# Kernel optimization log

Hardware: AMD Instinct MI355X
Metric: run time of the kernel (lower is better)

The kernel has to match this reference:

```python
import jax, jax.numpy as jnp
import numpy as np

B, L, C, N, TN = 1, 256, 128, 4, 4
CH = N * C  # 512, flattened hidden for routing projections
EPS = 1.1920929e-07  # torch.finfo(float32).eps (RMSNorm default eps)
LN_EPS = 1e-5
N_SINKHORN = 20  # training-mode iteration count


def sinkhorn_knopp(raw, n_iters):
    # raw: [..., n, n] real-valued logits -> doubly-stochastic matrix
    M = jnp.exp(raw)
    for _ in range(n_iters):
        M = M / jnp.sum(M, axis=-1, keepdims=True)  # row normalize
        M = M / jnp.sum(M, axis=-2, keepdims=True)  # col normalize
    return M


def setup_inputs() -> dict:
    key = jax.random.key(0)
    ks = jax.random.split(key, 8)
    s = 0.02
    eye = jnp.eye(N, dtype=jnp.float32)
    b_res = 2.0 * eye + (-2.0) * (1.0 - eye)
    return {
        "p": jax.random.normal(ks[0], (B, L, L, C), jnp.float32),
        "p_mask": jnp.ones((B, L, L), jnp.float32),
        "W_pre": jax.random.normal(ks[1], (N, CH), jnp.float32) * s,
        "W_post": jax.random.normal(ks[2], (N, CH), jnp.float32) * s,
        "W_res": jax.random.normal(ks[3], (N * N, CH), jnp.float32) * s,
        "b_pre": jnp.zeros((1, N), jnp.float32),
        "b_post": jnp.zeros((1, N), jnp.float32),
        "b_res": b_res,
        "alpha_pre": jnp.asarray(0.01, jnp.float32),
        "alpha_post": jnp.asarray(0.01, jnp.float32),
        "alpha_res": jnp.asarray(0.01, jnp.float32),
        "ln_g": jnp.ones((C,), jnp.float32),
        "ln_b": jnp.zeros((C,), jnp.float32),
        "W1": jax.random.normal(ks[4], (TN * C, C), jnp.float32) * s,
        "b1": jnp.zeros((TN * C,), jnp.float32),
        "W2": jax.random.normal(ks[5], (C, TN * C), jnp.float32) * s,
        "b2": jnp.zeros((C,), jnp.float32),
    }


def reference(p, p_mask, W_pre, W_post, W_res, b_pre, b_post, b_res,
              alpha_pre, alpha_post, alpha_res, ln_g, ln_b, W1, b1, W2, b2):
    # expand_input: [B,L,L,C] -> [B,L,L,n,C]
    x = jnp.broadcast_to(p[..., None, :], (B, L, L, N, C))
    # --- compute_mappings ---
    xf = x.reshape(B, L, L, CH)
    xn = xf * jax.lax.rsqrt(jnp.mean(xf * xf, axis=-1, keepdims=True) + EPS)
    H_pre_dyn = jnp.tanh(xn @ W_pre.T)                      # [B,L,L,n]
    H_post_dyn = jnp.tanh(xn @ W_post.T)                    # [B,L,L,n]
    H_res_dyn = jnp.tanh(xn @ W_res.T).reshape(B, L, L, N, N)
    H_pre = jax.nn.sigmoid(alpha_pre * H_pre_dyn + b_pre)   # [B,L,L,n]
    H_post = 2.0 * jax.nn.sigmoid(alpha_post * H_post_dyn + b_post)
    H_res = sinkhorn_knopp(alpha_res * H_res_dyn + b_res, N_SINKHORN)  # [B,L,L,n,n]
    # contract: H_pre [B,L,L,1,n] @ x [B,L,L,n,C] -> [B,L,L,C]
    p_c = jnp.einsum('blkn,blknc->blkc', H_pre, x)
    # --- PairTransition (LN -> Linear -> ReLU -> Linear, masked) ---
    mu = jnp.mean(p_c, axis=-1, keepdims=True)
    var = jnp.mean(jnp.square(p_c - mu), axis=-1, keepdims=True)
    m = (p_c - mu) * jax.lax.rsqrt(var + LN_EPS) * ln_g + ln_b
    h = jax.nn.relu(m @ W1.T + b1)                          # [B,L,L,TN*C]
    p_t = (h @ W2.T + b2) * p_mask[..., None]
    p_updated = p_c + p_t
    # expand back: H_post^T [B,L,L,n,1] * p_updated [B,L,L,1,C]
    p_expanded = H_post[..., :, None] * p_updated[..., None, :]
    # residual mixing: [B,L,L,n,n] @ [B,L,L,n,C]
    p_residual = jnp.einsum('blkmn,blknc->blkmc', H_res, x)
    return p_residual + p_expanded  # [B,L,L,n,C]
```

## Files before the change

kernel.cpp:

```cpp
#include <hip/hip_runtime.h>
#include <stdint.h>

#define LLTOT 65536
#define CDIM  128
#define TPIX  32

typedef float f32x4 __attribute__((ext_vector_type(4)));
typedef short s16x8 __attribute__((ext_vector_type(8)));

#define MFMA16(a, b, c) __builtin_amdgcn_mfma_f32_16x16x32_bf16((a), (b), (c), 0, 0, 0)

__device__ __align__(16) unsigned short g_wefff[2 * 4 * 64 * 8];
__device__ __align__(16) unsigned short g_w1gf[32 * 4 * 64 * 8];
__device__ __align__(16) unsigned short g_w2f [8 * 16 * 64 * 8];
__device__ __align__(16) float  g_hA[512];
__device__ __align__(16) float  g_w1gs[512];

__device__ __forceinline__ unsigned short f2bf(float f) {
    union { float f; uint32_t u; } v; v.f = f;
    uint32_t u = v.u;
    return (unsigned short)((u + 0x7FFFu + ((u >> 16) & 1u)) >> 16);
}
__device__ __forceinline__ uint32_t pack2(float a, float b) {
    uint32_t r;
    asm("v_cvt_pk_bf16_f32 %0, %1, %2" : "=v"(r) : "v"(a), "v"(b));
    return r;
}
__device__ __forceinline__ float bf2f(uint32_t lo16) { return __uint_as_float(lo16 << 16); }

__device__ __forceinline__ float fast_tanh(float x) {
    float cx = fminf(fmaxf(x, -10.f), 10.f);
    float e = __expf(2.f * cx);
    return (e - 1.f) * __builtin_amdgcn_rcpf(e + 1.f);
}
__device__ __forceinline__ float fast_sig(float z) {
    return __builtin_amdgcn_rcpf(1.f + __expf(-z));
}

__global__ void prep_kernel(const float* __restrict__ Wpre, const float* __restrict__ Wpost,
                            const float* __restrict__ Wres, const float* __restrict__ W1,
                            const float* __restrict__ W2, const float* __restrict__ ln_g,
                            const float* __restrict__ ln_b, const float* __restrict__ b1) {
    int b = blockIdx.x, t = threadIdx.x;
    if (b == 264) {
        int j = t;
        float sg = 0.f, sb = 0.f;
        const float* row = W1 + j * 128;
        #pragma unroll 4
        for (int c = 0; c < 128; c += 4) {
            float4 wv = *(const float4*)(row + c);
            float4 gv = *(const float4*)(ln_g + c);
            float4 bv = *(const float4*)(ln_b + c);
            sg += wv.x*gv.x + wv.y*gv.y + wv.z*gv.z + wv.w*gv.w;
            sb += wv.x*bv.x + wv.y*bv.y + wv.z*bv.z + wv.w*bv.w;
        }
        g_hA[j]   = b1[j] + sb;
        g_w1gs[j] = sg;
        return;
    }
    int idx = b * 512 + t;
    if (idx < 4096) {
        int e = idx & 7, lane = (idx >> 3) & 63, kk = (idx >> 9) & 3, tile = idx >> 11;
        int o = tile * 16 + (lane & 15);
        int c = kk * 32 + (lane >> 4) * 8 + e;
        float v = 0.f;
        if (o < 4)        v = Wpre[o*512+c] + Wpre[o*512+128+c] + Wpre[o*512+256+c] + Wpre[o*512+384+c];
        else if (o < 8)   { int j = o - 4;  v = Wpost[j*512+c] + Wpost[j*512+128+c] + Wpost[j*512+256+c] + Wpost[j*512+384+c]; }
        else if (o < 24)  { int j = o - 8;  v = Wres[j*512+c] + Wres[j*512+128+c] + Wres[j*512+256+c] + Wres[j*512+384+c]; }
        g_wefff[idx] = f2bf(v);
    } else if (idx < 69632) {
        int d = idx - 4096;
        int e = d & 7, lane = (d >> 3) & 63, kk = (d >> 9) & 3, jt = d >> 11;
        int j = jt * 16 + (lane & 15);
        int c = kk * 32 + (lane >> 4) * 8 + e;
        g_w1gf[d] = f2bf(W1[j * 128 + c] * ln_g[c]);
    } else if (idx < 135168) {
        int d = idx - 69632;
        int e = d & 7, lane = (d >> 3) & 63, kk = (d >> 9) & 15, ct = d >> 13;
        int c = ct * 16 + (lane & 15);
        int k = kk * 32 + (lane >> 4) * 8 + e;
        g_w2f[d] = f2bf(W2[c * 512 + k]);
    }
}

__global__ void __launch_bounds__(512, 4) fused_kernel(
    const float* __restrict__ p, const float* __restrict__ p_mask,
    const float* __restrict__ b_pre, const float* __restrict__ b_post, const float* __restrict__ b_res,
    const float* __restrict__ a_pre, const float* __restrict__ a_post, const float* __restrict__ a_res,
    const float* __restrict__ b2g, float* __restrict__ out)
{
    __shared__ __align__(16) unsigned short pf_lds[8 * 64 * 8];
    __shared__ __align__(16) unsigned short h_s[TPIX * 256];
    __shared__ __align__(16) float A_s[TPIX * 4], B_s[TPIX * 4];
    __shared__ __align__(16) float2 simi_s[TPIX];

    const int t = threadIdx.x;
    const int w = t >> 6, l = t & 63, lr = l & 15, lk = l >> 4;
    const size_t base = (size_t)blockIdx.x * 32;

    if (w < 2) {
        const int g = lk, pixl = lr;
        const size_t gpix = base + w * 16 + pixl;

        float s = 0.f, ss = 0.f;
        s16x8 pf[4];
        const float* prow = p + gpix * 128 + g * 8;
        #pragma unroll
        for (int kk = 0; kk < 4; ++kk) {
            float4 va = *(const float4*)(prow + kk * 32);
            float4 vb = *(const float4*)(prow + kk * 32 + 4);
            s  += va.x + va.y + va.z + va.w + vb.x + vb.y + vb.z + vb.w;
            ss += va.x*va.x + va.y*va.y + va.z*va.z + va.w*va.w
                + vb.x*vb.x + vb.y*vb.y + vb.z*vb.z + vb.w*vb.w;
            union { s16x8 v; uint32_t u[4]; } cc;
            cc.u[0] = pack2(va.x, va.y);
            cc.u[1] = pack2(va.z, va.w);
            cc.u[2] = pack2(vb.x, vb.y);
            cc.u[3] = pack2(vb.z, vb.w);
            pf[kk] = cc.v;
            *(s16x8*)(pf_lds + (size_t)(w * 4 + kk) * 512 + l * 8) = cc.v;
        }
        s  += __shfl_xor(s, 16);  ss += __shfl_xor(ss, 16);
        s  += __shfl_xor(s, 32);  ss += __shfl_xor(ss, 32);
        float mu = s * (1.f / 128.f), mq = ss * (1.f / 128.f);
        float rv  = rsqrtf(mq + 1.1920929e-07f);
        float var = mq - mu * mu;

        f32x4 y1 = {0.f, 0.f, 0.f, 0.f}, y2 = {0.f, 0.f, 0.f, 0.f};
        #pragma unroll
        for (int kk = 0; kk < 4; ++kk) {
            s16x8 a0 = *(const s16x8*)(g_wefff + ((size_t)(kk) * 64 + l) * 8);
            s16x8 a1 = *(const s16x8*)(g_wefff + ((size_t)(4 + kk) * 64 + l) * 8);
            y1 = MFMA16(a0, pf[kk], y1);
            y2 = MFMA16(a1, pf[kk], y2);
        }
        #pragma unroll
        for (int r = 0; r < 4; ++r) { y1[r] *= rv; y2[r] *= rv; }

        float apre = a_pre[0], apost = a_post[0], ares = a_res[0];

        float sp_loc = 0.f;
        #pragma unroll
        for (int r = 0; r < 4; ++r)
            sp_loc += fast_sig(apre * fast_tanh(y1[r]) + b_pre[r]);
        float sp = __shfl(sp_loc, pixl);

        float hp0 = 2.f * fast_sig(apost * fast_tanh(y1[0]) + b_post[0]);
        float hp1 = 2.f * fast_sig(apost * fast_tanh(y1[1]) + b_post[1]);
        float hp2 = 2.f * fast_sig(apost * fast_tanh(y1[2]) + b_post[2]);
        float hp3 = 2.f * fast_sig(apost * fast_tanh(y1[3]) + b_post[3]);

        int m = (g + 2) & 3;
        bool lo = g < 2;
        float M0 = __expf(ares * fast_tanh(lo ? y2[0] : y1[0]) + b_res[m * 4 + 0]);
        float M1 = __expf(ares * fast_tanh(lo ? y2[1] : y1[1]) + b_res[m * 4 + 1]);
        float M2 = __expf(ares * fast_tanh(lo ? y2[2] : y1[2]) + b_res[m * 4 + 2]);
        float M3 = __expf(ares * fast_tanh(lo ? y2[3] : y1[3]) + b_res[m * 4 + 3]);
        #pragma unroll 1
        for (int it = 0; it < 20; ++it) {
            float ri = __builtin_amdgcn_rcpf(M0 + M1 + M2 + M3);
            M0 *= ri; M1 *= ri; M2 *= ri; M3 *= ri;
            float c0 = M0, c1 = M1, c2 = M2, c3 = M3;
            c0 += __shfl_xor(c0, 16); c1 += __shfl_xor(c1, 16); c2 += __shfl_xor(c2, 16); c3 += __shfl_xor(c3, 16);
            c0 += __shfl_xor(c0, 32); c1 += __shfl_xor(c1, 32); c2 += __shfl_xor(c2, 32); c3 += __shfl_xor(c3, 32);
            M0 *= __builtin_amdgcn_rcpf(c0); M1 *= __builtin_amdgcn_rcpf(c1);
            M2 *= __builtin_amdgcn_rcpf(c2); M3 *= __builtin_amdgcn_rcpf(c3);
        }
        float rm = M0 + M1 + M2 + M3;

        float h0b = __shfl(hp0, pixl + 16);
        float h1b = __shfl(hp1, pixl + 16);
        float h2b = __shfl(hp2, pixl + 16);
        float h3b = __shfl(hp3, pixl + 16);
        float hpm = (m & 2) ? ((m & 1) ? h3b : h2b) : ((m & 1) ? h1b : h0b);

        float msk = p_mask[gpix];
        int pix = w * 16 + pixl;
        A_s[pix * 4 + m] = rm + hpm * sp;
        B_s[pix * 4 + m] = hpm * msk;
        if (l < 16) {
            float istd = rsqrtf(sp * sp * var + 1e-5f);
            simi_s[pix] = make_float2(sp * istd, sp * mu * istd);
        }
    }
    __syncthreads();

    float2 sim0 = simi_s[lr];
    float2 sim1 = simi_s[16 + lr];

    f32x4 acc2[2] = {};

    auto mlp_phase = [&](int phase) {
        f32x4 acc1[2][2] = {};
        #pragma unroll
        for (int kk = 0; kk < 4; ++kk) {
            s16x8 b0 = *(const s16x8*)(pf_lds + (size_t)(kk) * 512 + l * 8);
            s16x8 b1 = *(const s16x8*)(pf_lds + (size_t)(4 + kk) * 512 + l * 8);
            #pragma unroll
            for (int jt = 0; jt < 2; ++jt) {
                int T = phase * 16 + w * 2 + jt;
                s16x8 a = *(const s16x8*)(g_w1gf + ((size_t)(T * 4 + kk) * 64 + l) * 8);
                acc1[jt][0] = MFMA16(a, b0, acc1[jt][0]);
                acc1[jt][1] = MFMA16(a, b1, acc1[jt][1]);
            }
        }
        #pragma unroll
        for (int jt = 0; jt < 2; ++jt) {
            int jl = w * 32 + jt * 16 + lk * 4;
            int j0 = phase * 256 + jl;
            float4 wg = *(const float4*)(g_w1gs + j0);
            float4 ha = *(const float4*)(g_hA + j0);
            #pragma unroll
            for (int it = 0; it < 2; ++it) {
                int i = it * 16 + lr;
                float si = it ? sim1.x : sim0.x;
                float mi = it ? sim1.y : sim0.y;
                f32x4 v = acc1[jt][it];
                float h0 = fmaxf(fmaf(si, v[0], fmaf(-mi, wg.x, ha.x)), 0.f);
                float h1 = fmaxf(fmaf(si, v[1], fmaf(-mi, wg.y, ha.y)), 0.f);
                float h2 = fmaxf(fmaf(si, v[2], fmaf(-mi, wg.z, ha.z)), 0.f);
                float h3 = fmaxf(fmaf(si, v[3], fmaf(-mi, wg.w, ha.w)), 0.f);
                uint2 uu;
                uu.x = pack2(h0, h1);
                uu.y = pack2(h2, h3);
                uint32_t off = (uint32_t)(i * 512 + jl * 2) ^ ((i & 7) << 5);
                *(uint2*)((char*)h_s + off) = uu;
            }
        }
        __syncthreads();
        #pragma unroll
        for (int kk = 0; kk < 8; ++kk) {
            int K = phase * 8 + kk;
            s16x8 a = *(const s16x8*)(g_w2f + ((size_t)(w * 16 + K) * 64 + l) * 8);
            s16x8 b0, b1;
            {
                uint32_t off = (uint32_t)(lr * 512 + kk * 64 + lk * 16) ^ ((lr & 7) << 5);
                b0 = *(const s16x8*)((const char*)h_s + off);
            }
            {
                int i = 16 + lr;
                uint32_t off = (uint32_t)(i * 512 + kk * 64 + lk * 16) ^ ((i & 7) << 5);
                b1 = *(const s16x8*)((const char*)h_s + off);
            }
            acc2[0] = MFMA16(a, b0, acc2[0]);
            acc2[1] = MFMA16(a, b1, acc2[1]);
        }
    };

    mlp_phase(0);
    __syncthreads();
    mlp_phase(1);

    const int c0 = w * 16 + lk * 4;
    float4 b2v = *(const float4*)(b2g + c0);
    #pragma unroll
    for (int it = 0; it < 2; ++it) {
        int i = it * 16 + lr;
        f32x4 Av = *(const f32x4*)(A_s + i * 4);
        f32x4 Bv = *(const f32x4*)(B_s + i * 4);
        const unsigned short* pe = pf_lds
            + ((size_t)(it * 4 + (w >> 1)) * 64 + ((w & 1) * 2 + (lk >> 1)) * 16 + lr) * 8
            + (lk & 1) * 4;
        uint2 pb = *(const uint2*)pe;
        float p0 = bf2f(pb.x & 0xffffu), p1 = __uint_as_float(pb.x & 0xffff0000u);
        float p2 = bf2f(pb.y & 0xffffu), p3 = __uint_as_float(pb.y & 0xffff0000u);
        float d0 = acc2[it][0] + b2v.x, d1 = acc2[it][1] + b2v.y;
        float d2 = acc2[it][2] + b2v.z, d3 = acc2[it][3] + b2v.w;
        float* og = out + (base + i) * 512 + c0;
        #pragma unroll
        for (int m = 0; m < 4; ++m) {
            f32x4 o;
            o[0] = Av[m] * p0 + Bv[m] * d0;
            o[1] = Av[m] * p1 + Bv[m] * d1;
            o[2] = Av[m] * p2 + Bv[m] * d2;
            o[3] = Av[m] * p3 + Bv[m] * d3;
            *(f32x4*)(og + m * 128) = o;
        }
    }
}

extern "C" void kernel_launch(void* const* d_in, const int* in_sizes, int n_in,
                              void* d_out, int out_size, void* d_ws, size_t ws_size,
                              hipStream_t stream) {
    const float* p      = (const float*)d_in[0];
    const float* p_mask = (const float*)d_in[1];
    const float* W_pre  = (const float*)d_in[2];
    const float* W_post = (const float*)d_in[3];
    const float* W_res  = (const float*)d_in[4];
    const float* b_pre  = (const float*)d_in[5];
    const float* b_post = (const float*)d_in[6];
    const float* b_res  = (const float*)d_in[7];
    const float* a_pre  = (const float*)d_in[8];
    const float* a_post = (const float*)d_in[9];
    const float* a_res  = (const float*)d_in[10];
    const float* ln_g   = (const float*)d_in[11];
    const float* ln_b   = (const float*)d_in[12];
    const float* W1     = (const float*)d_in[13];
    const float* b1     = (const float*)d_in[14];
    const float* W2     = (const float*)d_in[15];
    const float* b2     = (const float*)d_in[16];
    float* out = (float*)d_out;

    prep_kernel<<<265, 512, 0, stream>>>(W_pre, W_post, W_res, W1, W2, ln_g, ln_b, b1);
    fused_kernel<<<2048, 512, 0, stream>>>(p, p_mask, b_pre, b_post, b_res,
                                           a_pre, a_post, a_res, b2, out);
}
```

Measured before the change: 75.46 us.

## Use 32x32 MFMA with split-K for second GEMM and single-phase first GEMM

```diff
diff --git a/kernel.cpp b/kernel.cpp
--- a/kernel.cpp
+++ b/kernel.cpp
@@ -5,14 +5,16 @@
 #define CDIM  128
 #define TPIX  32
 
-typedef float f32x4 __attribute__((ext_vector_type(4)));
-typedef short s16x8 __attribute__((ext_vector_type(8)));
+typedef float f32x4  __attribute__((ext_vector_type(4)));
+typedef float f32x16 __attribute__((ext_vector_type(16)));
+typedef short s16x8  __attribute__((ext_vector_type(8)));
 
 #define MFMA16(a, b, c) __builtin_amdgcn_mfma_f32_16x16x32_bf16((a), (b), (c), 0, 0, 0)
+#define MFMA32(a, b, c) __builtin_amdgcn_mfma_f32_32x32x16_bf16((a), (b), (c), 0, 0, 0)
 
 __device__ __align__(16) unsigned short g_wefff[2 * 4 * 64 * 8];
 __device__ __align__(16) unsigned short g_w1gf[32 * 4 * 64 * 8];
-__device__ __align__(16) unsigned short g_w2f [8 * 16 * 64 * 8];
+__device__ __align__(16) unsigned short g_w2f [4 * 32 * 64 * 8];
 __device__ __align__(16) float  g_hA[512];
 __device__ __align__(16) float  g_w1gs[512];
 
@@ -76,31 +78,41 @@
         g_w1gf[d] = f2bf(W1[j * 128 + c] * ln_g[c]);
     } else if (idx < 135168) {
         int d = idx - 69632;
-        int e = d & 7, lane = (d >> 3) & 63, kk = (d >> 9) & 15, ct = d >> 13;
-        int c = ct * 16 + (lane & 15);
-        int k = kk * 32 + (lane >> 4) * 8 + e;
+        int e = d & 7, lane = (d >> 3) & 63, kk = (d >> 9) & 31, ct = (d >> 14) & 3;
+        int c = ct * 32 + (lane & 31);
+        int k = kk * 16 + (lane >> 5) * 8 + e;
         g_w2f[d] = f2bf(W2[c * 512 + k]);
     }
 }
 
-__global__ void __launch_bounds__(512, 4) fused_kernel(
+__global__ void __launch_bounds__(512, 2) fused_kernel(
     const float* __restrict__ p, const float* __restrict__ p_mask,
     const float* __restrict__ b_pre, const float* __restrict__ b_post, const float* __restrict__ b_res,
     const float* __restrict__ a_pre, const float* __restrict__ a_post, const float* __restrict__ a_res,
     const float* __restrict__ b2g, float* __restrict__ out)
 {
     __shared__ __align__(16) unsigned short pf_lds[8 * 64 * 8];
-    __shared__ __align__(16) unsigned short h_s[TPIX * 256];
-    __shared__ __align__(16) float A_s[TPIX * 4], B_s[TPIX * 4];
-    __shared__ __align__(16) float2 simi_s[TPIX];
+    __shared__ __align__(16) unsigned short h32[32 * 64 * 8];
+    __shared__ __align__(16) float red_s[4096];
+    __shared__ __align__(16) float A_s[128], B_s[128];
+    __shared__ __align__(16) float2 simi_s[32];
 
     const int t = threadIdx.x;
     const int w = t >> 6, l = t & 63, lr = l & 15, lk = l >> 4;
-    const size_t base = (size_t)blockIdx.x * 32;
+    const size_t base = (size_t)blockIdx.x * TPIX;
+
+    float M0 = 0.f, M1 = 0.f, M2 = 0.f, M3 = 0.f, sp = 0.f, hpm = 0.f;
+    int mrow = 0, pix = 0;
 
     if (w < 2) {
         const int g = lk, pixl = lr;
         const size_t gpix = base + w * 16 + pixl;
+        float apre = a_pre[0], apost = a_post[0], ares = a_res[0];
+        float msk = p_mask[gpix];
+        float bp0 = b_pre[0], bp1 = b_pre[1], bp2 = b_pre[2], bp3 = b_pre[3];
+        float bq0 = b_post[0], bq1 = b_post[1], bq2 = b_post[2], bq3 = b_post[3];
+        mrow = (g + 2) & 3;
+        float br0 = b_res[mrow*4+0], br1 = b_res[mrow*4+1], br2 = b_res[mrow*4+2], br3 = b_res[mrow*4+3];
 
         float s = 0.f, ss = 0.f;
         s16x8 pf[4];
@@ -137,25 +149,39 @@
         #pragma unroll
         for (int r = 0; r < 4; ++r) { y1[r] *= rv; y2[r] *= rv; }
 
-        float apre = a_pre[0], apost = a_post[0], ares = a_res[0];
-
-        float sp_loc = 0.f;
-        #pragma unroll
-        for (int r = 0; r < 4; ++r)
-            sp_loc += fast_sig(apre * fast_tanh(y1[r]) + b_pre[r]);
-        float sp = __shfl(sp_loc, pixl);
-
-        float hp0 = 2.f * fast_sig(apost * fast_tanh(y1[0]) + b_post[0]);
-        float hp1 = 2.f * fast_sig(apost * fast_tanh(y1[1]) + b_post[1]);
-        float hp2 = 2.f * fast_sig(apost * fast_tanh(y1[2]) + b_post[2]);
-        float hp3 = 2.f * fast_sig(apost * fast_tanh(y1[3]) + b_post[3]);
-
-        int m = (g + 2) & 3;
+        float sp_loc = fast_sig(apre * fast_tanh(y1[0]) + bp0)
+                     + fast_sig(apre * fast_tanh(y1[1]) + bp1)
+                     + fast_sig(apre * fast_tanh(y1[2]) + bp2)
+                     + fast_sig(apre * fast_tanh(y1[3]) + bp3);
+        sp = __shfl(sp_loc, pixl);
+
+        float hp0 = 2.f * fast_sig(apost * fast_tanh(y1[0]) + bq0);
+        float hp1 = 2.f * fast_sig(apost * fast_tanh(y1[1]) + bq1);
+        float hp2 = 2.f * fast_sig(apost * fast_tanh(y1[2]) + bq2);
+        float hp3 = 2.f * fast_sig(apost * fast_tanh(y1[3]) + bq3);
+
         bool lo = g < 2;
-        float M0 = __expf(ares * fast_tanh(lo ? y2[0] : y1[0]) + b_res[m * 4 + 0]);
-        float M1 = __expf(ares * fast_tanh(lo ? y2[1] : y1[1]) + b_res[m * 4 + 1]);
-        float M2 = __expf(ares * fast_tanh(lo ? y2[2] : y1[2]) + b_res[m * 4 + 2]);
-        float M3 = __expf(ares * fast_tanh(lo ? y2[3] : y1[3]) + b_res[m * 4 + 3]);
+        M0 = __expf(ares * fast_tanh(lo ? y2[0] : y1[0]) + br0);
+        M1 = __expf(ares * fast_tanh(lo ? y2[1] : y1[1]) + br1);
+        M2 = __expf(ares * fast_tanh(lo ? y2[2] : y1[2]) + br2);
+        M3 = __expf(ares * fast_tanh(lo ? y2[3] : y1[3]) + br3);
+
+        float h0b = __shfl(hp0, pixl + 16);
+        float h1b = __shfl(hp1, pixl + 16);
+        float h2b = __shfl(hp2, pixl + 16);
+        float h3b = __shfl(hp3, pixl + 16);
+        hpm = (mrow & 2) ? ((mrow & 1) ? h3b : h2b) : ((mrow & 1) ? h1b : h0b);
+
+        pix = w * 16 + pixl;
+        B_s[pix * 4 + mrow] = hpm * msk;
+        if (l < 16) {
+            float istd = rsqrtf(sp * sp * var + 1e-5f);
+            simi_s[pix] = make_float2(sp * istd, sp * mu * istd);
+        }
+    }
+    __syncthreads();
+
+    if (w < 2) {
         #pragma unroll 1
         for (int it = 0; it < 20; ++it) {
             float ri = __builtin_amdgcn_rcpf(M0 + M1 + M2 + M3);
@@ -167,52 +193,36 @@
             M2 *= __builtin_amdgcn_rcpf(c2); M3 *= __builtin_amdgcn_rcpf(c3);
         }
         float rm = M0 + M1 + M2 + M3;
-
-        float h0b = __shfl(hp0, pixl + 16);
-        float h1b = __shfl(hp1, pixl + 16);
-        float h2b = __shfl(hp2, pixl + 16);
-        float h3b = __shfl(hp3, pixl + 16);
-        float hpm = (m & 2) ? ((m & 1) ? h3b : h2b) : ((m & 1) ? h1b : h0b);
-
-        float msk = p_mask[gpix];
-        int pix = w * 16 + pixl;
-        A_s[pix * 4 + m] = rm + hpm * sp;
-        B_s[pix * 4 + m] = hpm * msk;
-        if (l < 16) {
-            float istd = rsqrtf(sp * sp * var + 1e-5f);
-            simi_s[pix] = make_float2(sp * istd, sp * mu * istd);
-        }
-    }
-    __syncthreads();
-
-    float2 sim0 = simi_s[lr];
-    float2 sim1 = simi_s[16 + lr];
-
-    f32x4 acc2[2] = {};
-
-    auto mlp_phase = [&](int phase) {
-        f32x4 acc1[2][2] = {};
-        #pragma unroll
-        for (int kk = 0; kk < 4; ++kk) {
-            s16x8 b0 = *(const s16x8*)(pf_lds + (size_t)(kk) * 512 + l * 8);
-            s16x8 b1 = *(const s16x8*)(pf_lds + (size_t)(4 + kk) * 512 + l * 8);
-            #pragma unroll
-            for (int jt = 0; jt < 2; ++jt) {
-                int T = phase * 16 + w * 2 + jt;
-                s16x8 a = *(const s16x8*)(g_w1gf + ((size_t)(T * 4 + kk) * 64 + l) * 8);
-                acc1[jt][0] = MFMA16(a, b0, acc1[jt][0]);
-                acc1[jt][1] = MFMA16(a, b1, acc1[jt][1]);
-            }
-        }
-        #pragma unroll
-        for (int jt = 0; jt < 2; ++jt) {
-            int jl = w * 32 + jt * 16 + lk * 4;
-            int j0 = phase * 256 + jl;
+        A_s[pix * 4 + mrow] = rm + hpm * sp;
+    }
+
+    s16x8 pfr[2][4];
+    #pragma unroll
+    for (int it = 0; it < 2; ++it)
+        #pragma unroll
+        for (int kk = 0; kk < 4; ++kk)
+            pfr[it][kk] = *(const s16x8*)(pf_lds + (size_t)(it * 4 + kk) * 512 + l * 8);
+
+    f32x4 acc1[4][2] = {};
+    #pragma unroll
+    for (int kk = 0; kk < 4; ++kk)
+        #pragma unroll
+        for (int jt = 0; jt < 4; ++jt) {
+            s16x8 a = *(const s16x8*)(g_w1gf + ((size_t)((w * 4 + jt) * 4 + kk) * 64 + l) * 8);
+            acc1[jt][0] = MFMA16(a, pfr[0][kk], acc1[jt][0]);
+            acc1[jt][1] = MFMA16(a, pfr[1][kk], acc1[jt][1]);
+        }
+
+    {
+        float2 sim0 = simi_s[lr];
+        float2 sim1 = simi_s[16 + lr];
+        #pragma unroll
+        for (int jt = 0; jt < 4; ++jt) {
+            int j0 = w * 64 + jt * 16 + lk * 4;
             float4 wg = *(const float4*)(g_w1gs + j0);
             float4 ha = *(const float4*)(g_hA + j0);
             #pragma unroll
             for (int it = 0; it < 2; ++it) {
-                int i = it * 16 + lr;
                 float si = it ? sim1.x : sim0.x;
                 float mi = it ? sim1.y : sim0.y;
                 f32x4 v = acc1[jt][it];
@@ -223,58 +233,61 @@
                 uint2 uu;
                 uu.x = pack2(h0, h1);
                 uu.y = pack2(h2, h3);
-                uint32_t off = (uint32_t)(i * 512 + jl * 2) ^ ((i & 7) << 5);
-                *(uint2*)((char*)h_s + off) = uu;
+                uint32_t addr = (uint32_t)((w * 4 + jt) * 1024
+                              + (it * 16 + lr + 32 * (lk >> 1)) * 16 + (lk & 1) * 8);
+                *(uint2*)((char*)h32 + addr) = uu;
             }
         }
-        __syncthreads();
-        #pragma unroll
-        for (int kk = 0; kk < 8; ++kk) {
-            int K = phase * 8 + kk;
-            s16x8 a = *(const s16x8*)(g_w2f + ((size_t)(w * 16 + K) * 64 + l) * 8);
-            s16x8 b0, b1;
-            {
-                uint32_t off = (uint32_t)(lr * 512 + kk * 64 + lk * 16) ^ ((lr & 7) << 5);
-                b0 = *(const s16x8*)((const char*)h_s + off);
-            }
-            {
-                int i = 16 + lr;
-                uint32_t off = (uint32_t)(i * 512 + kk * 64 + lk * 16) ^ ((i & 7) << 5);
-                b1 = *(const s16x8*)((const char*)h_s + off);
-            }
-            acc2[0] = MFMA16(a, b0, acc2[0]);
-            acc2[1] = MFMA16(a, b1, acc2[1]);
-        }
-    };
-
-    mlp_phase(0);
+    }
     __syncthreads();
-    mlp_phase(1);
-
-    const int c0 = w * 16 + lk * 4;
-    float4 b2v = *(const float4*)(b2g + c0);
-    #pragma unroll
-    for (int it = 0; it < 2; ++it) {
-        int i = it * 16 + lr;
+
+    const int ct = w & 3, kh = w >> 2;
+    f32x16 acc2 = {0.f,0.f,0.f,0.f, 0.f,0.f,0.f,0.f, 0.f,0.f,0.f,0.f, 0.f,0.f,0.f,0.f};
+    #pragma unroll 4
+    for (int kk2 = 0; kk2 < 16; ++kk2) {
+        int ks = kh * 16 + kk2;
+        s16x8 a = *(const s16x8*)(g_w2f + ((size_t)(ct * 32 + ks) * 64 + l) * 8);
+        s16x8 b = *(const s16x8*)(h32 + (size_t)ks * 512 + l * 8);
+        acc2 = MFMA32(a, b, acc2);
+    }
+    if (kh) {
+        #pragma unroll
+        for (int q = 0; q < 4; ++q) {
+            f32x4 v = {acc2[4*q+0], acc2[4*q+1], acc2[4*q+2], acc2[4*q+3]};
+            *(f32x4*)(red_s + ct * 1024 + q * 256 + l * 4) = v;
+        }
+    }
+    __syncthreads();
+
+    if (w < 4) {
+        int i = l & 31;
         f32x4 Av = *(const f32x4*)(A_s + i * 4);
         f32x4 Bv = *(const f32x4*)(B_s + i * 4);
-        const unsigned short* pe = pf_lds
-            + ((size_t)(it * 4 + (w >> 1)) * 64 + ((w & 1) * 2 + (lk >> 1)) * 16 + lr) * 8
-            + (lk & 1) * 4;
-        uint2 pb = *(const uint2*)pe;
-        float p0 = bf2f(pb.x & 0xffffu), p1 = __uint_as_float(pb.x & 0xffff0000u);
-        float p2 = bf2f(pb.y & 0xffffu), p3 = __uint_as_float(pb.y & 0xffff0000u);
-        float d0 = acc2[it][0] + b2v.x, d1 = acc2[it][1] + b2v.y;
-        float d2 = acc2[it][2] + b2v.z, d3 = acc2[it][3] + b2v.w;
-        float* og = out + (base + i) * 512 + c0;
-        #pragma unroll
-        for (int m = 0; m < 4; ++m) {
-            f32x4 o;
-            o[0] = Av[m] * p0 + Bv[m] * d0;
-            o[1] = Av[m] * p1 + Bv[m] * d1;
-            o[2] = Av[m] * p2 + Bv[m] * d2;
-            o[3] = Av[m] * p3 + Bv[m] * d3;
-            *(f32x4*)(og + m * 128) = o;
+        #pragma unroll
+        for (int q = 0; q < 4; ++q) {
+            f32x4 r4 = *(const f32x4*)(red_s + ct * 1024 + q * 256 + l * 4);
+            int cb = ct * 32 + 8 * q + 4 * (l >> 5);
+            float4 b2v = *(const float4*)(b2g + cb);
+            float d0 = acc2[4*q+0] + r4[0] + b2v.x;
+            float d1 = acc2[4*q+1] + r4[1] + b2v.y;
+            float d2 = acc2[4*q+2] + r4[2] + b2v.z;
+            float d3 = acc2[4*q+3] + r4[3] + b2v.w;
+            const unsigned short* pe = pf_lds
+                + (size_t)(((l >> 4) & 1) * 4 + ct) * 512
+                + ((l & 15) + 16 * q) * 8 + (l >> 5) * 4;
+            uint2 pb = *(const uint2*)pe;
+            float p0 = bf2f(pb.x & 0xffffu), p1 = __uint_as_float(pb.x & 0xffff0000u);
+            float p2 = bf2f(pb.y & 0xffffu), p3 = __uint_as_float(pb.y & 0xffff0000u);
+            float* og = out + (base + i) * 512 + cb;
+            #pragma unroll
+            for (int m = 0; m < 4; ++m) {
+                f32x4 o;
+                o[0] = Av[m] * p0 + Bv[m] * d0;
+                o[1] = Av[m] * p1 + Bv[m] * d1;
+                o[2] = Av[m] * p2 + Bv[m] * d2;
+                o[3] = Av[m] * p3 + Bv[m] * d3;
+                *(f32x4*)(og + m * 128) = o;
+            }
         }
     }
 }
```

Result: slower. 87.09 us (+15.4%).
